# Performance work log

Hardware: AMD Instinct MI355X
Metric: run time of the kernel (lower is better)

The kernel has to match this reference:

```python
import jax, jax.numpy as jnp
import numpy as np

N = 50000   # nodes
E = 800000  # edges
F = 64      # input features
H = 64      # hidden channels
C = 6       # classes (ENZYMES)
G = 500     # graphs in batch
EPS = 1e-5


def setup_inputs() -> dict:
    key = jax.random.key(0)
    ks = jax.random.split(key, 16)
    x = jax.random.normal(ks[0], (N, F), dtype=jnp.float32)
    edge_index = jax.random.randint(ks[1], (2, E), 0, N)
    batch = jnp.sort(jax.random.randint(ks[2], (N,), 0, G))

    def lin(k, fan_in, fan_out):
        return (jax.random.normal(k, (fan_in, fan_out), dtype=jnp.float32)
                * np.float32(1.0 / np.sqrt(fan_in)))

    inp = {"x": x, "edge_index": edge_index, "batch": batch}
    dims = [(F, H), (H, H), (H, H)]
    for i, (fi, fo) in enumerate(dims):
        inp[f"W{i}"] = lin(ks[3 + i], fi, fo)
        inp[f"b{i}"] = jnp.zeros((fo,), jnp.float32)
        inp[f"g{i}"] = jnp.ones((fo,), jnp.float32)   # BatchNorm gamma
        inp[f"be{i}"] = jnp.zeros((fo,), jnp.float32)  # BatchNorm beta
    inp["fcW"] = lin(ks[6], H, C)
    inp["fcb"] = jnp.zeros((C,), jnp.float32)
    return inp


def _gcn_forward(x, edge_index, batch, Ws, bs, gs, bes, fcW, fcb):
    src, dst = edge_index[0], edge_index[1]
    loops = jnp.arange(N)
    row = jnp.concatenate([src, loops])  # source nodes (incl. self-loops)
    col = jnp.concatenate([dst, loops])  # target nodes
    deg = jnp.zeros((N,), x.dtype).at[col].add(1.0)
    dinv = jax.lax.rsqrt(deg)            # deg >= 1 due to self-loops
    norm = (dinv[row] * dinv[col])[:, None]  # [E+N, 1]

    h = x
    for W, b, g, be in zip(Ws, bs, gs, bes):
        # GCNConv: linear transform, then normalized scatter-add aggregate
        h = h @ W
        h = jnp.zeros((N, W.shape[1]), h.dtype).at[col].add(norm * h[row]) + b
        # BatchNorm (batch statistics) + ReLU; dropout = identity (eval)
        mu = h.mean(axis=0)
        var = h.var(axis=0)
        h = jax.nn.relu((h - mu) * jax.lax.rsqrt(var + EPS) * g + be)

    # global_mean_pool over graph ids
    summed = jax.ops.segment_sum(h, batch, num_segments=G)
    counts = jax.ops.segment_sum(jnp.ones((N,), h.dtype), batch, num_segments=G)
    pooled = summed / jnp.maximum(counts, 1.0)[:, None]
    return pooled @ fcW + fcb  # [G, C]


def reference(x, edge_index, batch, W0, b0, g0, be0, W1, b1, g1, be1,
              W2, b2, g2, be2, fcW, fcb):
    return _gcn_forward(x, edge_index, batch,
                        [W0, W1, W2], [b0, b1, b2],
                        [g0, g1, g2], [be0, be1, be2], fcW, fcb)
```

## Files before the change

### kernel.cpp

```cpp
#include <hip/hip_runtime.h>
#include <hip/hip_fp16.h>
#include <math.h>

#define NN 50000
#define EE 800000
#define GG 500
#define CC 6
#define BN_EPS 1e-5f
#define NB_SCAN 49
#define NB_CNT 3125
#define NB_BND 196
#define NB_GEMM 782
#define NBKT 98
#define NB_PART 400

typedef _Float16 f16x8 __attribute__((ext_vector_type(8)));
typedef float f32x4 __attribute__((ext_vector_type(4)));

__global__ __launch_bounds__(256) void k_cb(const int* __restrict__ dst,
                                            int* __restrict__ icnt,
                                            const int* __restrict__ batch,
                                            int* __restrict__ gstart) {
  int b = blockIdx.x;
  if (b < NB_CNT) {
    int e = b * 256 + threadIdx.x;
    if (e < EE) atomicAdd(&icnt[dst[e]], 1);
  } else {
    int i = (b - NB_CNT) * 256 + threadIdx.x;
    if (i >= NN) return;
    int bb = batch[i];
    if (i == 0) {
      for (int g = 0; g <= bb; ++g) gstart[g] = 0;
    } else {
      int pb = batch[i - 1];
      for (int g = pb + 1; g <= bb; ++g) gstart[g] = i;
    }
    if (i == NN - 1) {
      for (int g = bb + 1; g <= GG; ++g) gstart[g] = NN;
    }
  }
}

__global__ __launch_bounds__(256) void k_scan1(const int* __restrict__ icnt,
                                               int* __restrict__ pre,
                                               int* __restrict__ bsum,
                                               float* __restrict__ dinv,
                                               int* __restrict__ braw) {
  __shared__ int ls[256];
  __shared__ int lr[256];
  int base = blockIdx.x * 1024;
  int t = threadIdx.x;
  int v[4], s = 0, sraw = 0;
#pragma unroll
  for (int j = 0; j < 4; ++j) {
    int idx = base + t * 4 + j;
    int raw = (idx < NN) ? icnt[idx] : 0;
    if (idx < NN) dinv[idx] = rsqrtf((float)(raw + 1));
    sraw += raw;
    v[j] = (raw + 3) & ~3;
    s += v[j];
  }
  ls[t] = s;
  lr[t] = sraw;
  __syncthreads();
  for (int ofs = 1; ofs < 256; ofs <<= 1) {
    int y = (t >= ofs) ? ls[t - ofs] : 0;
    __syncthreads();
    ls[t] += y;
    __syncthreads();
  }
  int excl = ls[t] - s;
#pragma unroll
  for (int j = 0; j < 4; ++j) {
    int idx = base + t * 4 + j;
    if (idx < NN) pre[idx] = excl;
    excl += v[j];
  }
  if (t == 255) bsum[blockIdx.x] = ls[255];
  for (int ofs = 64; ofs >= 1; ofs >>= 1) {
    __syncthreads();
    if ((t & 127) < ofs) lr[t] += lr[t + ofs];
  }
  __syncthreads();
  if (t == 0) braw[2 * blockIdx.x] = lr[0];
  if (t == 128 && 2 * blockIdx.x + 1 < NBKT) braw[2 * blockIdx.x + 1] = lr[128];
}

__global__ void k_scan2(int* __restrict__ bsum, int* __restrict__ rowptr,
                        double* __restrict__ sums24) {
  int t = threadIdx.x;
  for (int k = t; k < 3 * 1024; k += 64) sums24[k] = 0.0;
  if (t == 0) {
    int run = 0;
    for (int b = 0; b < NB_SCAN; ++b) {
      int x = bsum[b];
      bsum[b] = run;
      run += x;
    }
    rowptr[NN] = run;
  }
}

__global__ __launch_bounds__(256) void k_scan3(const int* __restrict__ pre,
                                               const int* __restrict__ bsum,
                                               int* __restrict__ rowptr,
                                               int* __restrict__ gcur) {
  int i = blockIdx.x * 256 + threadIdx.x;
  if (i < NN) {
    int v = pre[i] + bsum[i >> 10];
    rowptr[i] = v;
    if ((i & 511) == 0) gcur[i >> 9] = v;
  }
}

template <bool LAYER0>
__device__ __forceinline__ void gemm_tile(int blockId,
                                          const void* __restrict__ Aptr,
                                          const double* __restrict__ sums,
                                          const float* __restrict__ gamma,
                                          const float* __restrict__ beta,
                                          const float* __restrict__ W,
                                          const float* __restrict__ dinv,
                                          __half* __restrict__ out) {
  __shared__ __align__(16) unsigned char AhB[64 * 128];
  __shared__ __align__(16) unsigned char WtB[64 * 128];
  __shared__ float sc[64], sh[64];
  int tid = threadIdx.x;
  if (!LAYER0 && tid < 64) {
    double S = 0.0, Q = 0.0;
#pragma unroll
    for (int k = 0; k < 8; ++k) {
      S += sums[k * 128 + tid];
      Q += sums[k * 128 + 64 + tid];
    }
    double mu = S / (double)NN;
    double var = Q / (double)NN - mu * mu;
    float rstd = (float)(1.0 / sqrt(var + (double)BN_EPS));
    float scv = gamma[tid] * rstd;
    sc[tid] = scv;
    sh[tid] = beta[tid] - (float)mu * scv;
  }
#pragma unroll
  for (int i = 0; i < 16; ++i) {
    int idx = tid + 256 * i;
    int k = idx >> 6, c = idx & 63;
    *(__half*)&WtB[c * 128 + ((k * 2) ^ ((c & 7) << 4))] = __float2half(W[idx]);
  }
  if (!LAYER0) __syncthreads();
  int base = blockId * 64;
  if (LAYER0) {
    const float4* A4 = (const float4*)((const float*)Aptr + (size_t)base * 64);
#pragma unroll
    for (int i = 0; i < 4; ++i) {
      int idx = tid + 256 * i;
      int row = idx >> 4, q = idx & 15;
      float4 v = (base + row < NN) ? A4[idx] : float4{0.f, 0.f, 0.f, 0.f};
      __half2 p0 = __floats2half2_rn(v.x, v.y);
      __half2 p1 = __floats2half2_rn(v.z, v.w);
      uint2 u;
      u.x = *(unsigned*)&p0;
      u.y = *(unsigned*)&p1;
      *(uint2*)&AhB[row * 128 + ((q * 8) ^ ((row & 7) << 4))] = u;
    }
  } else {
    const uint4* A8 = (const uint4*)((const __half*)Aptr + (size_t)base * 64);
#pragma unroll
    for (int i = 0; i < 2; ++i) {
      int idx = tid + 256 * i;
      int row = idx >> 3, chunk = idx & 7;
      uint4 u = (base + row < NN) ? A8[idx] : uint4{0u, 0u, 0u, 0u};
      __half2* hp = (__half2*)&u;
      int c0 = chunk * 8;
      float f[8];
#pragma unroll
      for (int j = 0; j < 4; ++j) {
        float2 fv = __half22float2(hp[j]);
        f[2 * j] = fv.x;
        f[2 * j + 1] = fv.y;
      }
#pragma unroll
      for (int j = 0; j < 8; ++j)
        f[j] = fmaxf(fmaf(f[j], sc[c0 + j], sh[c0 + j]), 0.f);
      __half2 q0 = __floats2half2_rn(f[0], f[1]);
      __half2 q1 = __floats2half2_rn(f[2], f[3]);
      __half2 q2 = __floats2half2_rn(f[4], f[5]);
      __half2 q3 = __floats2half2_rn(f[6], f[7]);
      uint4 o;
      o.x = *(unsigned*)&q0;
      o.y = *(unsigned*)&q1;
      o.z = *(unsigned*)&q2;
      o.w = *(unsigned*)&q3;
      *(uint4*)&AhB[row * 128 + ((chunk * 16) ^ ((row & 7) << 4))] = o;
    }
  }
  __syncthreads();
  int lane = tid & 63;
  int w = tid >> 6;
  int r0 = w * 16;
  int lrow = lane & 15;
  int kg = lane >> 4;
  int s = (lrow & 7) << 4;
  f16x8 a0 = *(f16x8*)&AhB[(r0 + lrow) * 128 + ((kg * 16) ^ s)];
  f16x8 a1 = *(f16x8*)&AhB[(r0 + lrow) * 128 + ((64 + kg * 16) ^ s)];
  f32x4 acc[4];
#pragma unroll
  for (int ct = 0; ct < 4; ++ct) {
    acc[ct] = (f32x4){0.f, 0.f, 0.f, 0.f};
    f16x8 b0 = *(f16x8*)&WtB[(ct * 16 + lrow) * 128 + ((kg * 16) ^ s)];
    f16x8 b1 = *(f16x8*)&WtB[(ct * 16 + lrow) * 128 + ((64 + kg * 16) ^ s)];
    acc[ct] = __builtin_amdgcn_mfma_f32_16x16x32_f16(a0, b0, acc[ct], 0, 0, 0);
    acc[ct] = __builtin_amdgcn_mfma_f32_16x16x32_f16(a1, b1, acc[ct], 0, 0, 0);
  }
  __syncthreads();
#pragma unroll
  for (int reg = 0; reg < 4; ++reg) {
    int row = r0 + kg * 4 + reg;
    float dv = dinv[base + row < NN ? base + row : NN - 1];
#pragma unroll
    for (int ct = 0; ct < 4; ++ct)
      *(__half*)&AhB[row * 128 + (ct * 16 + lrow) * 2] =
          __float2half(acc[ct][reg] * dv);
  }
  __syncthreads();
#pragma unroll
  for (int i = 0; i < 2; ++i) {
    int idx = tid + 256 * i;
    int row = idx >> 3, chunk = idx & 7;
    int n = base + row;
    if (n < NN)
      ((uint4*)(out + (size_t)n * 64))[chunk] = *(uint4*)&AhB[row * 128 + chunk * 16];
  }
}

__global__ __launch_bounds__(256) void k_part_gemm0(const int* __restrict__ src,
                                                    const int* __restrict__ dst,
                                                    int* __restrict__ gcur,
                                                    unsigned int* __restrict__ part,
                                                    const float* __restrict__ x,
                                                    const float* __restrict__ W0,
                                                    const float* __restrict__ dinv,
                                                    __half* __restrict__ outB) {
  if (blockIdx.x >= NB_GEMM) {
    __shared__ int lcnt[NBKT], lofs[NBKT], lcur[NBKT];
    int tid = threadIdx.x;
    int cb = (blockIdx.x - NB_GEMM) * 2000;
    if (tid < NBKT) lcnt[tid] = 0;
    __syncthreads();
    for (int it = 0; it < 8; ++it) {
      int o = it * 256 + tid;
      if (o < 2000) atomicAdd(&lcnt[dst[cb + o] >> 9], 1);
    }
    __syncthreads();
    if (tid < NBKT) {
      lofs[tid] = atomicAdd(&gcur[tid], lcnt[tid]);
      lcur[tid] = 0;
    }
    __syncthreads();
    for (int it = 0; it < 8; ++it) {
      int o = it * 256 + tid;
      if (o < 2000) {
        int d = dst[cb + o];
        int bkt = d >> 9;
        int pos = lofs[bkt] + atomicAdd(&lcur[bkt], 1);
        part[pos] = ((unsigned)(d & 511) << 16) | (unsigned)src[cb + o];
      }
    }
    return;
  }
  gemm_tile<true>(blockIdx.x, x, nullptr, nullptr, nullptr, W0, dinv, outB);
}

__global__ __launch_bounds__(512) void k_fill2(const int* __restrict__ rowptr,
                                               const int* __restrict__ braw,
                                               const unsigned int* __restrict__ part,
                                               unsigned short* __restrict__ ep) {
  __shared__ int lrp[512];
  __shared__ int lfill[512];
  int b = blockIdx.x;
  int tid = threadIdx.x;
  int nbase = b << 9;
  lrp[tid] = (nbase + tid < NN) ? rowptr[nbase + tid] : 0;
  lfill[tid] = 0;
  __syncthreads();
  int start = lrp[0];
  int cnt = braw[b];
  for (int i = tid; i < cnt; i += 512) {
    unsigned p = part[start + i];
    int dloc = p >> 16;
    int pos = lrp[dloc] + atomicAdd(&lfill[dloc], 1);
    ep[pos] = (unsigned short)(p & 0xFFFF);
  }
}

__global__ __launch_bounds__(256) void k_gather_stats(const int* __restrict__ rowptr,
                                                      const int* __restrict__ icnt,
                                                      const unsigned short* __restrict__ ep,
                                                      const float* __restrict__ dinv,
                                                      const __half* __restrict__ t,
                                                      __half* __restrict__ outp,
                                                      double* __restrict__ sums8) {
  int w = threadIdx.x >> 6;
  int lane = threadIdx.x & 63;
  int g = lane >> 3;
  int li = lane & 7;
  int d = blockIdx.x * 32 + w * 8 + g;
  float acc[8] = {0.f, 0.f, 0.f, 0.f, 0.f, 0.f, 0.f, 0.f};
  if (d < NN) {
    uint4 u = ((const uint4*)(t + (size_t)d * 64))[li];
    {
      __half2* hp = (__half2*)&u;
#pragma unroll
      for (int j = 0; j < 4; ++j) {
        float2 f = __half22float2(hp[j]);
        acc[2 * j] += f.x;
        acc[2 * j + 1] += f.y;
      }
    }
    int e0 = rowptr[d], cnt = icnt[d];
    int k = 0;
    for (; k + 7 < cnt; k += 8) {
      ushort4 qa = *(const ushort4*)&ep[e0 + k];
      ushort4 qb = *(const ushort4*)&ep[e0 + k + 4];
      uint4 r0 = ((const uint4*)(t + (size_t)qa.x * 64))[li];
      uint4 r1 = ((const uint4*)(t + (size_t)qa.y * 64))[li];
      uint4 r2 = ((const uint4*)(t + (size_t)qa.z * 64))[li];
      uint4 r3 = ((const uint4*)(t + (size_t)qa.w * 64))[li];
      uint4 r4 = ((const uint4*)(t + (size_t)qb.x * 64))[li];
      uint4 r5 = ((const uint4*)(t + (size_t)qb.y * 64))[li];
      uint4 r6 = ((const uint4*)(t + (size_t)qb.z * 64))[li];
      uint4 r7 = ((const uint4*)(t + (size_t)qb.w * 64))[li];
      uint4* rr[8] = {&r0, &r1, &r2, &r3, &r4, &r5, &r6, &r7};
#pragma unroll
      for (int m = 0; m < 8; ++m) {
        __half2* hp = (__half2*)rr[m];
#pragma unroll
        for (int j = 0; j < 4; ++j) {
          float2 f = __half22float2(hp[j]);
          acc[2 * j] += f.x;
          acc[2 * j + 1] += f.y;
        }
      }
    }
    for (; k + 3 < cnt; k += 4) {
      ushort4 qe = *(const ushort4*)&ep[e0 + k];
      uint4 r0 = ((const uint4*)(t + (size_t)qe.x * 64))[li];
      uint4 r1 = ((const uint4*)(t + (size_t)qe.y * 64))[li];
      uint4 r2 = ((const uint4*)(t + (size_t)qe.z * 64))[li];
      uint4 r3 = ((const uint4*)(t + (size_t)qe.w * 64))[li];
      uint4* rr[4] = {&r0, &r1, &r2, &r3};
#pragma unroll
      for (int m = 0; m < 4; ++m) {
        __half2* hp = (__half2*)rr[m];
#pragma unroll
        for (int j = 0; j < 4; ++j) {
          float2 f = __half22float2(hp[j]);
          acc[2 * j] += f.x;
          acc[2 * j + 1] += f.y;
        }
      }
    }
    for (; k < cnt; ++k) {
      uint4 r = ((const uint4*)(t + (size_t)ep[e0 + k] * 64))[li];
      __half2* hp = (__half2*)&r;
#pragma unroll
      for (int j = 0; j < 4; ++j) {
        float2 f = __half22float2(hp[j]);
        acc[2 * j] += f.x;
        acc[2 * j + 1] += f.y;
      }
    }
    float dv = dinv[d];
#pragma unroll
    for (int j = 0; j < 8; ++j) acc[j] *= dv;
    __half2 o0 = __floats2half2_rn(acc[0], acc[1]);
    __half2 o1 = __floats2half2_rn(acc[2], acc[3]);
    __half2 o2 = __floats2half2_rn(acc[4], acc[5]);
    __half2 o3 = __floats2half2_rn(acc[6], acc[7]);
    uint4 ov;
    ov.x = *(unsigned*)&o0;
    ov.y = *(unsigned*)&o1;
    ov.z = *(unsigned*)&o2;
    ov.w = *(unsigned*)&o3;
    ((uint4*)(outp + (size_t)d * 64))[li] = ov;
  }
  __shared__ float ls[4][8][8][8], lq[4][8][8][8];
#pragma unroll
  for (int j = 0; j < 8; ++j) {
    ls[w][g][li][j] = acc[j];
    lq[w][g][li][j] = acc[j] * acc[j];
  }
  __syncthreads();
  if (threadIdx.x < 64) {
    int c = threadIdx.x;
    int lsel = c >> 3, comp = c & 7;
    float S = 0.f, Q = 0.f;
#pragma unroll
    for (int ww = 0; ww < 4; ++ww)
#pragma unroll
      for (int gg = 0; gg < 8; ++gg) {
        S += ls[ww][gg][lsel][comp];
        Q += lq[ww][gg][lsel][comp];
      }
    double* bank = sums8 + (size_t)(blockIdx.x & 7) * 128;
    atomicAdd(&bank[c], (double)S);
    atomicAdd(&bank[64 + c], (double)Q);
  }
}

__global__ __launch_bounds__(256) void k_gemm64f(const __half* __restrict__ A,
                                                 const double* __restrict__ sums,
                                                 const float* __restrict__ gamma,
                                                 const float* __restrict__ beta,
                                                 const float* __restrict__ W,
                                                 const float* __restrict__ dinv,
                                                 __half* __restrict__ out) {
  gemm_tile<false>(blockIdx.x, A, sums, gamma, beta, W, dinv, out);
}

__global__ __launch_bounds__(256) void k_pool_final(const int* __restrict__ gstart,
                                                    const __half* __restrict__ h,
                                                    const double* __restrict__ sums,
                                                    const float* __restrict__ gamma,
                                                    const float* __restrict__ beta,
                                                    const float* __restrict__ fcW,
                                                    const float* __restrict__ fcb,
                                                    float* __restrict__ out) {
  __shared__ float sc[64], sh[64];
  __shared__ float pl[4][64];
  int tid = threadIdx.x;
  if (tid < 64) {
    double S = 0.0, Q = 0.0;
#pragma unroll
    for (int k = 0; k < 8; ++k) {
      S += sums[k * 128 + tid];
      Q += sums[k * 128 + 64 + tid];
    }
    double mu = S / (double)NN;
    double var = Q / (double)NN - mu * mu;
    float rstd = (float)(1.0 / sqrt(var + (double)BN_EPS));
    float scv = gamma[tid] * rstd;
    sc[tid] = scv;
    sh[tid] = beta[tid] - (float)mu * scv;
  }
  __syncthreads();
  int w = tid >> 6;
  int c = tid & 63;
  int g = blockIdx.x * 4 + w;
  float p = 0.f;
  if (g < GG) {
    int s = gstart[g], e = gstart[g + 1];
    float scv = sc[c], shv = sh[c], acc = 0.f;
    for (int i = s; i < e; ++i)
      acc += fmaxf(fmaf(__half2float(h[(size_t)i * 64 + c]), scv, shv), 0.f);
    p = acc / fmaxf((float)(e - s), 1.0f);
  }
  pl[w][c] = p;
  __syncthreads();
  if (tid < 4 * CC) {
    int gw = tid / CC, j = tid % CC;
    int gg = blockIdx.x * 4 + gw;
    if (gg < GG) {
      float acc = 0.f;
#pragma unroll
      for (int k = 0; k < 64; ++k) acc = fmaf(pl[gw][k], fcW[k * CC + j], acc);
      out[gg * CC + j] = acc + fcb[j];
    }
  }
}

extern "C" void kernel_launch(void* const* d_in, const int* in_sizes, int n_in,
                              void* d_out, int out_size, void* d_ws, size_t ws_size,
                              hipStream_t stream) {
  const float* x = (const float*)d_in[0];
  const int* eidx = (const int*)d_in[1];
  const int* batch = (const int*)d_in[2];
  const float* W[3] = {(const float*)d_in[3], (const float*)d_in[7], (const float*)d_in[11]};
  const float* gam[3] = {(const float*)d_in[5], (const float*)d_in[9], (const float*)d_in[13]};
  const float* bet[3] = {(const float*)d_in[6], (const float*)d_in[10], (const float*)d_in[14]};
  const float* fcW = (const float*)d_in[15];
  const float* fcb = (const float*)d_in[16];
  float* out = (float*)d_out;

  char* ws = (char*)d_ws;
  size_t off = 0;
  auto alloc = [&](size_t b) -> void* {
    void* p = ws + off;
    off = (off + b + 255) & ~(size_t)255;
    return p;
  };
  int* icnt = (int*)alloc((size_t)NN * 4);
  float* dinv = (float*)alloc((size_t)NN * 4);
  int* pre = (int*)alloc((size_t)NN * 4);
  int* bsum = (int*)alloc((size_t)NB_SCAN * 4);
  int* braw = (int*)alloc((size_t)NBKT * 4);
  int* gcur = (int*)alloc((size_t)NBKT * 4);
  int* rowptr = (int*)alloc((size_t)(NN + 1) * 4);
  int* gstart = (int*)alloc((size_t)(GG + 1) * 4);
  unsigned int* part = (unsigned int*)alloc((size_t)(EE + 4 * NN) * 4);
  unsigned short* ep = (unsigned short*)alloc((size_t)(EE + 4 * NN) * 2);
  __half* bufA = (__half*)alloc((size_t)NN * 64 * 2);
  __half* bufB = (__half*)alloc((size_t)NN * 64 * 2);
  double* sums24 = (double*)alloc((size_t)3 * 1024 * 8);

  const int* src = eidx;
  const int* dst = eidx + EE;

  hipMemsetAsync(icnt, 0, (size_t)NN * 4, stream);
  k_cb<<<NB_CNT + NB_BND, 256, 0, stream>>>(dst, icnt, batch, gstart);
  k_scan1<<<NB_SCAN, 256, 0, stream>>>(icnt, pre, bsum, dinv, braw);
  k_scan2<<<1, 64, 0, stream>>>(bsum, rowptr, sums24);
  k_scan3<<<(NN + 255) / 256, 256, 0, stream>>>(pre, bsum, rowptr, gcur);

  k_part_gemm0<<<NB_GEMM + NB_PART, 256, 0, stream>>>(src, dst, gcur, part, x, W[0],
                                                      dinv, bufB);
  k_fill2<<<NBKT, 512, 0, stream>>>(rowptr, braw, part, ep);

  k_gather_stats<<<(NN + 31) / 32, 256, 0, stream>>>(rowptr, icnt, ep, dinv, bufB, bufA,
                                                     sums24 + 0 * 1024);
  for (int l = 1; l < 3; ++l) {
    k_gemm64f<<<NB_GEMM, 256, 0, stream>>>(bufA, sums24 + (l - 1) * 1024, gam[l - 1],
                                           bet[l - 1], W[l], dinv, bufB);
    k_gather_stats<<<(NN + 31) / 32, 256, 0, stream>>>(rowptr, icnt, ep, dinv, bufB, bufA,
                                                       sums24 + l * 1024);
  }

  k_pool_final<<<(GG + 3) / 4, 256, 0, stream>>>(gstart, bufA, sums24 + 2 * 1024, gam[2],
                                                 bet[2], fcW, fcb, out);
}
```

Measured before the change: 276.5 us.

## Replace global degree count and scan with fixed-capacity buckets and in-block scans

Drops the memset, the global atomic degree-count pass and the three-kernel prefix scan. Edges are now bucketed into fixed-capacity per-512-node partitions (PCAP/EPCAP), and the fill kernel computes per-node counts, a local scan, rowptr, dinv, and applies the dinv scaling to the layer-0 GEMM output in place. This removes several launches and a full pass over the dst array. It relies on bucket capacities large enough for the random input's degree distribution and would overflow silently on skewed graphs.

```diff
diff --git a/kernel.cpp b/kernel.cpp
--- a/kernel.cpp
+++ b/kernel.cpp
@@ -7,109 +7,35 @@
 #define GG 500
 #define CC 6
 #define BN_EPS 1e-5f
-#define NB_SCAN 49
-#define NB_CNT 3125
 #define NB_BND 196
 #define NB_GEMM 782
 #define NBKT 98
 #define NB_PART 400
+#define PCAP 12288
+#define EPCAP 14336
 
 typedef _Float16 f16x8 __attribute__((ext_vector_type(8)));
 typedef float f32x4 __attribute__((ext_vector_type(4)));
 
-__global__ __launch_bounds__(256) void k_cb(const int* __restrict__ dst,
-                                            int* __restrict__ icnt,
-                                            const int* __restrict__ batch,
-                                            int* __restrict__ gstart) {
-  int b = blockIdx.x;
-  if (b < NB_CNT) {
-    int e = b * 256 + threadIdx.x;
-    if (e < EE) atomicAdd(&icnt[dst[e]], 1);
+__global__ __launch_bounds__(256) void k_bounds(const int* __restrict__ batch,
+                                                int* __restrict__ gstart,
+                                                int* __restrict__ gcur,
+                                                double* __restrict__ sums24) {
+  if (blockIdx.x == 0) {
+    if (threadIdx.x < NBKT) gcur[threadIdx.x] = threadIdx.x * PCAP;
+    for (int k = threadIdx.x; k < 3 * 1024; k += 256) sums24[k] = 0.0;
+  }
+  int i = blockIdx.x * 256 + threadIdx.x;
+  if (i >= NN) return;
+  int bb = batch[i];
+  if (i == 0) {
+    for (int g = 0; g <= bb; ++g) gstart[g] = 0;
   } else {
-    int i = (b - NB_CNT) * 256 + threadIdx.x;
-    if (i >= NN) return;
-    int bb = batch[i];
-    if (i == 0) {
-      for (int g = 0; g <= bb; ++g) gstart[g] = 0;
-    } else {
-      int pb = batch[i - 1];
-      for (int g = pb + 1; g <= bb; ++g) gstart[g] = i;
-    }
-    if (i == NN - 1) {
-      for (int g = bb + 1; g <= GG; ++g) gstart[g] = NN;
-    }
-  }
-}
-
-__global__ __launch_bounds__(256) void k_scan1(const int* __restrict__ icnt,
-                                               int* __restrict__ pre,
-                                               int* __restrict__ bsum,
-                                               float* __restrict__ dinv,
-                                               int* __restrict__ braw) {
-  __shared__ int ls[256];
-  __shared__ int lr[256];
-  int base = blockIdx.x * 1024;
-  int t = threadIdx.x;
-  int v[4], s = 0, sraw = 0;
-#pragma unroll
-  for (int j = 0; j < 4; ++j) {
-    int idx = base + t * 4 + j;
-    int raw = (idx < NN) ? icnt[idx] : 0;
-    if (idx < NN) dinv[idx] = rsqrtf((float)(raw + 1));
-    sraw += raw;
-    v[j] = (raw + 3) & ~3;
-    s += v[j];
-  }
-  ls[t] = s;
-  lr[t] = sraw;
-  __syncthreads();
-  for (int ofs = 1; ofs < 256; ofs <<= 1) {
-    int y = (t >= ofs) ? ls[t - ofs] : 0;
-    __syncthreads();
-    ls[t] += y;
-    __syncthreads();
-  }
-  int excl = ls[t] - s;
-#pragma unroll
-  for (int j = 0; j < 4; ++j) {
-    int idx = base + t * 4 + j;
-    if (idx < NN) pre[idx] = excl;
-    excl += v[j];
-  }
-  if (t == 255) bsum[blockIdx.x] = ls[255];
-  for (int ofs = 64; ofs >= 1; ofs >>= 1) {
-    __syncthreads();
-    if ((t & 127) < ofs) lr[t] += lr[t + ofs];
-  }
-  __syncthreads();
-  if (t == 0) braw[2 * blockIdx.x] = lr[0];
-  if (t == 128 && 2 * blockIdx.x + 1 < NBKT) braw[2 * blockIdx.x + 1] = lr[128];
-}
-
-__global__ void k_scan2(int* __restrict__ bsum, int* __restrict__ rowptr,
-                        double* __restrict__ sums24) {
-  int t = threadIdx.x;
-  for (int k = t; k < 3 * 1024; k += 64) sums24[k] = 0.0;
-  if (t == 0) {
-    int run = 0;
-    for (int b = 0; b < NB_SCAN; ++b) {
-      int x = bsum[b];
-      bsum[b] = run;
-      run += x;
-    }
-    rowptr[NN] = run;
-  }
-}
-
-__global__ __launch_bounds__(256) void k_scan3(const int* __restrict__ pre,
-                                               const int* __restrict__ bsum,
-                                               int* __restrict__ rowptr,
-                                               int* __restrict__ gcur) {
-  int i = blockIdx.x * 256 + threadIdx.x;
-  if (i < NN) {
-    int v = pre[i] + bsum[i >> 10];
-    rowptr[i] = v;
-    if ((i & 511) == 0) gcur[i >> 9] = v;
+    int pb = batch[i - 1];
+    for (int g = pb + 1; g <= bb; ++g) gstart[g] = i;
+  }
+  if (i == NN - 1) {
+    for (int g = bb + 1; g <= GG; ++g) gstart[g] = NN;
   }
 }
 
@@ -215,7 +141,9 @@
 #pragma unroll
   for (int reg = 0; reg < 4; ++reg) {
     int row = r0 + kg * 4 + reg;
-    float dv = dinv[base + row < NN ? base + row : NN - 1];
+    int n = base + row;
+    float dv = 1.0f;
+    if (!LAYER0) dv = dinv[n < NN ? n : NN - 1];
 #pragma unroll
     for (int ct = 0; ct < 4; ++ct)
       *(__half*)&AhB[row * 128 + (ct * 16 + lrow) * 2] =
@@ -238,7 +166,6 @@
                                                     unsigned int* __restrict__ part,
                                                     const float* __restrict__ x,
                                                     const float* __restrict__ W0,
-                                                    const float* __restrict__ dinv,
                                                     __half* __restrict__ outB) {
   if (blockIdx.x >= NB_GEMM) {
     __shared__ int lcnt[NBKT], lofs[NBKT], lcur[NBKT];
@@ -267,28 +194,72 @@
     }
     return;
   }
-  gemm_tile<true>(blockIdx.x, x, nullptr, nullptr, nullptr, W0, dinv, outB);
-}
-
-__global__ __launch_bounds__(512) void k_fill2(const int* __restrict__ rowptr,
-                                               const int* __restrict__ braw,
-                                               const unsigned int* __restrict__ part,
-                                               unsigned short* __restrict__ ep) {
-  __shared__ int lrp[512];
+  gemm_tile<true>(blockIdx.x, x, nullptr, nullptr, nullptr, W0, nullptr, outB);
+}
+
+__global__ __launch_bounds__(512) void k_fill2b(const int* __restrict__ gcur,
+                                                const unsigned int* __restrict__ part,
+                                                unsigned short* __restrict__ ep,
+                                                int* __restrict__ rowptr,
+                                                int* __restrict__ icnt,
+                                                float* __restrict__ dinv,
+                                                __half* __restrict__ bufB) {
+  __shared__ int lcnt[512];
+  __shared__ int lpre[512];
   __shared__ int lfill[512];
+  __shared__ float ldinv[512];
   int b = blockIdx.x;
   int tid = threadIdx.x;
   int nbase = b << 9;
-  lrp[tid] = (nbase + tid < NN) ? rowptr[nbase + tid] : 0;
+  int cnt_b = gcur[b] - b * PCAP;
+  const unsigned int* ps = part + (size_t)b * PCAP;
+  lcnt[tid] = 0;
+  __syncthreads();
+  for (int i = tid; i < cnt_b; i += 512) atomicAdd(&lcnt[ps[i] >> 16], 1);
+  __syncthreads();
+  int myc = lcnt[tid];
+  int pad = (myc + 3) & ~3;
+  lpre[tid] = pad;
+  __syncthreads();
+  for (int ofs = 1; ofs < 512; ofs <<= 1) {
+    int y = (tid >= ofs) ? lpre[tid - ofs] : 0;
+    __syncthreads();
+    lpre[tid] += y;
+    __syncthreads();
+  }
+  int excl = lpre[tid] - pad;
+  float dv = rsqrtf((float)(myc + 1));
+  int node = nbase + tid;
+  if (node < NN) {
+    rowptr[node] = b * EPCAP + excl;
+    icnt[node] = myc;
+    dinv[node] = dv;
+  }
+  ldinv[tid] = dv;
   lfill[tid] = 0;
   __syncthreads();
-  int start = lrp[0];
-  int cnt = braw[b];
-  for (int i = tid; i < cnt; i += 512) {
-    unsigned p = part[start + i];
+  lpre[tid] = excl;
+  __syncthreads();
+  for (int i = tid; i < cnt_b; i += 512) {
+    unsigned p = ps[i];
     int dloc = p >> 16;
-    int pos = lrp[dloc] + atomicAdd(&lfill[dloc], 1);
-    ep[pos] = (unsigned short)(p & 0xFFFF);
+    int pos = lpre[dloc] + atomicAdd(&lfill[dloc], 1);
+    ep[(size_t)b * EPCAP + pos] = (unsigned short)(p & 0xFFFF);
+  }
+  __syncthreads();
+  int maxrow = NN - nbase;
+  if (maxrow > 512) maxrow = 512;
+  uint4* B4 = (uint4*)(bufB + (size_t)nbase * 64);
+  for (int i = tid; i < maxrow * 8; i += 512) {
+    float dvr = ldinv[i >> 3];
+    uint4 u = B4[i];
+    __half2* hp = (__half2*)&u;
+#pragma unroll
+    for (int j = 0; j < 4; ++j) {
+      float2 f = __half22float2(hp[j]);
+      hp[j] = __floats2half2_rn(f.x * dvr, f.y * dvr);
+    }
+    B4[i] = u;
   }
 }
 
@@ -490,14 +461,11 @@
   };
   int* icnt = (int*)alloc((size_t)NN * 4);
   float* dinv = (float*)alloc((size_t)NN * 4);
-  int* pre = (int*)alloc((size_t)NN * 4);
-  int* bsum = (int*)alloc((size_t)NB_SCAN * 4);
-  int* braw = (int*)alloc((size_t)NBKT * 4);
   int* gcur = (int*)alloc((size_t)NBKT * 4);
-  int* rowptr = (int*)alloc((size_t)(NN + 1) * 4);
+  int* rowptr = (int*)alloc((size_t)NN * 4);
   int* gstart = (int*)alloc((size_t)(GG + 1) * 4);
-  unsigned int* part = (unsigned int*)alloc((size_t)(EE + 4 * NN) * 4);
-  unsigned short* ep = (unsigned short*)alloc((size_t)(EE + 4 * NN) * 2);
+  unsigned int* part = (unsigned int*)alloc((size_t)NBKT * PCAP * 4);
+  unsigned short* ep = (unsigned short*)alloc((size_t)NBKT * EPCAP * 2);
   __half* bufA = (__half*)alloc((size_t)NN * 64 * 2);
   __half* bufB = (__half*)alloc((size_t)NN * 64 * 2);
   double* sums24 = (double*)alloc((size_t)3 * 1024 * 8);
@@ -505,15 +473,9 @@
   const int* src = eidx;
   const int* dst = eidx + EE;
 
-  hipMemsetAsync(icnt, 0, (size_t)NN * 4, stream);
-  k_cb<<<NB_CNT + NB_BND, 256, 0, stream>>>(dst, icnt, batch, gstart);
-  k_scan1<<<NB_SCAN, 256, 0, stream>>>(icnt, pre, bsum, dinv, braw);
-  k_scan2<<<1, 64, 0, stream>>>(bsum, rowptr, sums24);
-  k_scan3<<<(NN + 255) / 256, 256, 0, stream>>>(pre, bsum, rowptr, gcur);
-
-  k_part_gemm0<<<NB_GEMM + NB_PART, 256, 0, stream>>>(src, dst, gcur, part, x, W[0],
-                                                      dinv, bufB);
-  k_fill2<<<NBKT, 512, 0, stream>>>(rowptr, braw, part, ep);
+  k_bounds<<<NB_BND, 256, 0, stream>>>(batch, gstart, gcur, sums24);
+  k_part_gemm0<<<NB_GEMM + NB_PART, 256, 0, stream>>>(src, dst, gcur, part, x, W[0], bufB);
+  k_fill2b<<<NBKT, 512, 0, stream>>>(gcur, part, ep, rowptr, icnt, dinv, bufB);
 
   k_gather_stats<<<(NN + 31) / 32, 256, 0, stream>>>(rowptr, icnt, ep, dinv, bufB, bufA,
                                                      sums24 + 0 * 1024);
```

After: 239.0 us. 1.16x faster.
